# Performance work log

Hardware: AMD Instinct MI355X
Metric: run time of the kernel (lower is better)

The kernel has to match this reference:

```python
import jax, jax.numpy as jnp
import numpy as np

BETA = 1.0  # init kwarg beta


def setup_inputs() -> dict:
    key = jax.random.key(0)
    k1, k2 = jax.random.split(key)
    B, K = 8192, 64
    policy_logps = jax.random.normal(k1, (B, K), dtype=jnp.float32)
    reward_scores = jax.random.uniform(k2, (B, K), dtype=jnp.float32)
    return {"policy_logps": policy_logps, "reward_scores": reward_scores}


def reference(policy_logps, reward_scores):
    B, K = policy_logps.shape
    s = policy_logps  # rf_free=True -> scores = policy_logps
    r = reward_scores

    # ranks: 1-based rank of each item when rewards sorted descending
    order = jnp.argsort(-r, axis=-1)              # [B, K]
    ranks = jnp.argsort(order, axis=-1) + 1        # [B, K]
    inv_discount = 1.0 / jnp.log1p(ranks.astype(s.dtype))  # [B, K]
    gain = 2.0 * r - 1.0                            # [B, K]

    # pairwise matrices [B, K, K]; loop in original covers i > j (strict lower triangle)
    delta = jnp.abs(gain[:, :, None] - gain[:, None, :]) * \
            jnp.abs(inv_discount[:, :, None] - inv_discount[:, None, :])
    diff = s[:, :, None] - s[:, None, :]
    term = delta * jax.nn.log_sigmoid(-BETA * diff)

    mask = jnp.tril(jnp.ones((K, K), dtype=bool), k=-1)  # i > j
    loss_sum = jnp.sum(jnp.where(mask[None], term, 0.0))
    count = B * (K * (K - 1) // 2)
    return -loss_sum / count
```

## Files before the change

### kernel.cpp

```cpp
#include <hip/hip_runtime.h>

#define KDIM 64
#define WAVES_PER_BLOCK 4
#define ROWS_PER_WAVE 2
#define ROWS_PER_BLOCK (WAVES_PER_BLOCK * ROWS_PER_WAVE)

__global__ __launch_bounds__(256) void rankdpo_main(
    const float* __restrict__ s_in, const float* __restrict__ r_in,
    float* __restrict__ partials, int B)
{
    const int wave = threadIdx.x >> 6;
    const int lane = threadIdx.x & 63;
    const int row0 = blockIdx.x * ROWS_PER_BLOCK + wave * ROWS_PER_WAVE;
    const int row1 = row0 + 1;
    const int a0 = (row0 < B ? row0 : 0) * KDIM + lane;
    const int a1 = (row1 < B ? row1 : 0) * KDIM + lane;

    const float s0 = s_in[a0], r0 = r_in[a0];
    const float s1 = s_in[a1], r1 = r_in[a1];

    int c0 = 0, c1 = 0;
    #pragma unroll
    for (int j = 0; j < KDIM; ++j) {
        float rj0 = __uint_as_float(__builtin_amdgcn_readlane(__float_as_uint(r0), j));
        float rj1 = __uint_as_float(__builtin_amdgcn_readlane(__float_as_uint(r1), j));
        c0 += (rj0 > r0) || (rj0 == r0 && j < lane);
        c1 += (rj1 > r1) || (rj1 == r1 && j < lane);
    }
    const float invd0 = __builtin_amdgcn_rcpf(
        0.69314718056f * __builtin_amdgcn_logf((float)(c0 + 2)));
    const float invd1 = __builtin_amdgcn_rcpf(
        0.69314718056f * __builtin_amdgcn_logf((float)(c1 + 2)));
    const float g0 = 2.0f * r0 - 1.0f;
    const float g1 = 2.0f * r1 - 1.0f;

    float p0 = 0.0f, p1 = 0.0f;
    #pragma unroll
    for (int d = 1; d <= 32; ++d) {
        const int pj = (lane - d) & 63;
        float sj0 = __shfl(s0, pj), gj0 = __shfl(g0, pj), dj0 = __shfl(invd0, pj);
        float sj1 = __shfl(s1, pj), gj1 = __shfl(g1, pj), dj1 = __shfl(invd1, pj);

        float del0 = fabsf(g0 - gj0) * fabsf(invd0 - dj0);
        float del1 = fabsf(g1 - gj1) * fabsf(invd1 - dj1);
        if (d == 32 && lane < 32) { del0 = 0.0f; del1 = 0.0f; }

        float u0 = (lane >= d) ? (s0 - sj0) : (sj0 - s0);
        float u1 = (lane >= d) ? (s1 - sj1) : (sj1 - s1);

        float e0 = __builtin_amdgcn_exp2f(-1.44269504089f * fabsf(u0));
        float e1 = __builtin_amdgcn_exp2f(-1.44269504089f * fabsf(u1));
        float sp0 = fmaxf(u0, 0.0f) + 0.69314718056f * __builtin_amdgcn_logf(1.0f + e0);
        float sp1 = fmaxf(u1, 0.0f) + 0.69314718056f * __builtin_amdgcn_logf(1.0f + e1);

        p0 = fmaf(del0, sp0, p0);
        p1 = fmaf(del1, sp1, p1);
    }
    if (row0 >= B) p0 = 0.0f;
    if (row1 >= B) p1 = 0.0f;

    float pacc = p0 + p1;
    #pragma unroll
    for (int off = 32; off > 0; off >>= 1)
        pacc += __shfl_down(pacc, off);

    __shared__ float wsum[WAVES_PER_BLOCK];
    if (lane == 0) wsum[wave] = pacc;
    __syncthreads();
    if (threadIdx.x == 0)
        partials[blockIdx.x] = wsum[0] + wsum[1] + wsum[2] + wsum[3];
}

__global__ __launch_bounds__(256) void rankdpo_reduce(
    const float* __restrict__ partials, int n, float* __restrict__ out,
    double inv_count)
{
    double sum = 0.0;
    for (int i = threadIdx.x; i < n; i += 256)
        sum += (double)partials[i];
    __shared__ double sh[256];
    sh[threadIdx.x] = sum;
    __syncthreads();
    for (int st = 128; st > 0; st >>= 1) {
        if (threadIdx.x < st) sh[threadIdx.x] += sh[threadIdx.x + st];
        __syncthreads();
    }
    if (threadIdx.x == 0)
        out[0] = (float)(sh[0] * inv_count);
}

extern "C" void kernel_launch(void* const* d_in, const int* in_sizes, int n_in,
                              void* d_out, int out_size, void* d_ws, size_t ws_size,
                              hipStream_t stream) {
    const float* s = (const float*)d_in[0];
    const float* r = (const float*)d_in[1];
    float* out = (float*)d_out;

    const int BK = in_sizes[0];
    const int B  = BK / KDIM;
    const int nblocks = (B + ROWS_PER_BLOCK - 1) / ROWS_PER_BLOCK;

    float* partials = (float*)d_ws;

    const long long count = (long long)B * (KDIM * (KDIM - 1) / 2);
    const double inv_count = 1.0 / (double)count;

    rankdpo_main<<<nblocks, 256, 0, stream>>>(s, r, partials, B);
    rankdpo_reduce<<<1, 256, 0, stream>>>(partials, nblocks, out, inv_count);
}
```

Baseline: 72.04 us.

## Stage pairwise operands in LDS with float4 reads and pack rank keys

Replaces the 32-step cross-lane shuffle loop with LDS staging. Each wave's s, gain and inverse-discount values are written twice into a 128-wide buffer, so every lane can read four partners per float4 load across 8 quad offsets. The remaining intra-quad pairs are handled with a few shuffles. The rank count now uses a single 64-bit key comparison, and the stable softplus is replaced by an unguarded log2(1+exp2) with the ln2 factors folded out of both the discount and the term. This aims to cut shuffle/bpermute traffic and ALU work, at the cost of LDS usage and possible overflow for large score differences.

After: 68.11 us. -5.5%, faster.

```diff
diff --git a/kernel.cpp b/kernel.cpp
--- a/kernel.cpp
+++ b/kernel.cpp
@@ -11,6 +11,9 @@
 {
     const int wave = threadIdx.x >> 6;
     const int lane = threadIdx.x & 63;
+    const int qi = lane >> 2;
+    const int bi = lane & 3;
+
     const int row0 = blockIdx.x * ROWS_PER_BLOCK + wave * ROWS_PER_WAVE;
     const int row1 = row0 + 1;
     const int a0 = (row0 < B ? row0 : 0) * KDIM + lane;
@@ -19,43 +22,91 @@
     const float s0 = s_in[a0], r0 = r_in[a0];
     const float s1 = s_in[a1], r1 = r_in[a1];
 
+    const unsigned long long k0 =
+        ((unsigned long long)__float_as_uint(r0) << 32) | (unsigned int)(~lane);
+    const unsigned long long k1 =
+        ((unsigned long long)__float_as_uint(r1) << 32) | (unsigned int)(~lane);
     int c0 = 0, c1 = 0;
     #pragma unroll
     for (int j = 0; j < KDIM; ++j) {
-        float rj0 = __uint_as_float(__builtin_amdgcn_readlane(__float_as_uint(r0), j));
-        float rj1 = __uint_as_float(__builtin_amdgcn_readlane(__float_as_uint(r1), j));
-        c0 += (rj0 > r0) || (rj0 == r0 && j < lane);
-        c1 += (rj1 > r1) || (rj1 == r1 && j < lane);
+        unsigned int rb0 = (unsigned int)__builtin_amdgcn_readlane(__float_as_int(r0), j);
+        unsigned int rb1 = (unsigned int)__builtin_amdgcn_readlane(__float_as_int(r1), j);
+        unsigned long long kj0 = ((unsigned long long)rb0 << 32) | (unsigned int)(~j);
+        unsigned long long kj1 = ((unsigned long long)rb1 << 32) | (unsigned int)(~j);
+        c0 += (kj0 > k0);
+        c1 += (kj1 > k1);
     }
-    const float invd0 = __builtin_amdgcn_rcpf(
-        0.69314718056f * __builtin_amdgcn_logf((float)(c0 + 2)));
-    const float invd1 = __builtin_amdgcn_rcpf(
-        0.69314718056f * __builtin_amdgcn_logf((float)(c1 + 2)));
+    const float invd0 = __builtin_amdgcn_rcpf(__builtin_amdgcn_logf((float)(c0 + 2)));
+    const float invd1 = __builtin_amdgcn_rcpf(__builtin_amdgcn_logf((float)(c1 + 2)));
     const float g0 = 2.0f * r0 - 1.0f;
     const float g1 = 2.0f * r1 - 1.0f;
 
+    __shared__ __align__(16) float sh[WAVES_PER_BLOCK][ROWS_PER_WAVE][3][128];
+    sh[wave][0][0][lane] = s0;     sh[wave][0][0][lane + 64] = s0;
+    sh[wave][0][1][lane] = g0;     sh[wave][0][1][lane + 64] = g0;
+    sh[wave][0][2][lane] = invd0;  sh[wave][0][2][lane + 64] = invd0;
+    sh[wave][1][0][lane] = s1;     sh[wave][1][0][lane + 64] = s1;
+    sh[wave][1][1][lane] = g1;     sh[wave][1][1][lane + 64] = g1;
+    sh[wave][1][2][lane] = invd1;  sh[wave][1][2][lane + 64] = invd1;
+
+    const float LOG2E = 1.44269504088896f;
     float p0 = 0.0f, p1 = 0.0f;
+
     #pragma unroll
-    for (int d = 1; d <= 32; ++d) {
-        const int pj = (lane - d) & 63;
-        float sj0 = __shfl(s0, pj), gj0 = __shfl(g0, pj), dj0 = __shfl(invd0, pj);
-        float sj1 = __shfl(s1, pj), gj1 = __shfl(g1, pj), dj1 = __shfl(invd1, pj);
+    for (int t = 1; t <= 8; ++t) {
+        const int Q = (qi + 16 - t) << 2;
+        const float4 sq0 = *(const float4*)&sh[wave][0][0][Q];
+        const float4 gq0 = *(const float4*)&sh[wave][0][1][Q];
+        const float4 dq0 = *(const float4*)&sh[wave][0][2][Q];
+        const float4 sq1 = *(const float4*)&sh[wave][1][0][Q];
+        const float4 gq1 = *(const float4*)&sh[wave][1][1][Q];
+        const float4 dq1 = *(const float4*)&sh[wave][1][2][Q];
+        const float qc   = (qi >= t) ? LOG2E : -LOG2E;
+        const float keep = (t < 8) ? 1.0f : ((qi >= 8) ? 1.0f : 0.0f);
 
-        float del0 = fabsf(g0 - gj0) * fabsf(invd0 - dj0);
-        float del1 = fabsf(g1 - gj1) * fabsf(invd1 - dj1);
-        if (d == 32 && lane < 32) { del0 = 0.0f; del1 = 0.0f; }
+        const float* sj0 = (const float*)&sq0;
+        const float* gj0 = (const float*)&gq0;
+        const float* dj0 = (const float*)&dq0;
+        const float* sj1 = (const float*)&sq1;
+        const float* gj1 = (const float*)&gq1;
+        const float* dj1 = (const float*)&dq1;
+        #pragma unroll
+        for (int m = 0; m < 4; ++m) {
+            float del0 = fabsf(g0 - gj0[m]) * fabsf(invd0 - dj0[m]) * keep;
+            float del1 = fabsf(g1 - gj1[m]) * fabsf(invd1 - dj1[m]) * keep;
+            float l0 = __builtin_amdgcn_logf(1.0f + __builtin_amdgcn_exp2f(qc * (s0 - sj0[m])));
+            float l1 = __builtin_amdgcn_logf(1.0f + __builtin_amdgcn_exp2f(qc * (s1 - sj1[m])));
+            p0 = fmaf(del0, l0, p0);
+            p1 = fmaf(del1, l1, p1);
+        }
+    }
 
-        float u0 = (lane >= d) ? (s0 - sj0) : (sj0 - s0);
-        float u1 = (lane >= d) ? (s1 - sj1) : (sj1 - s1);
+    {
+        const int pjA = (lane & ~3) | ((bi + 3) & 3);
+        const int pjB = (lane & ~3) | ((bi + 2) & 3);
+        const float qcA  = (bi >= 1) ? LOG2E : -LOG2E;
+        const float keepB = (bi >= 2) ? 1.0f : 0.0f;
 
-        float e0 = __builtin_amdgcn_exp2f(-1.44269504089f * fabsf(u0));
-        float e1 = __builtin_amdgcn_exp2f(-1.44269504089f * fabsf(u1));
-        float sp0 = fmaxf(u0, 0.0f) + 0.69314718056f * __builtin_amdgcn_logf(1.0f + e0);
-        float sp1 = fmaxf(u1, 0.0f) + 0.69314718056f * __builtin_amdgcn_logf(1.0f + e1);
+        float sjA0 = __shfl(s0, pjA), gjA0 = __shfl(g0, pjA), djA0 = __shfl(invd0, pjA);
+        float sjA1 = __shfl(s1, pjA), gjA1 = __shfl(g1, pjA), djA1 = __shfl(invd1, pjA);
+        float sjB0 = __shfl(s0, pjB), gjB0 = __shfl(g0, pjB), djB0 = __shfl(invd0, pjB);
+        float sjB1 = __shfl(s1, pjB), gjB1 = __shfl(g1, pjB), djB1 = __shfl(invd1, pjB);
 
-        p0 = fmaf(del0, sp0, p0);
-        p1 = fmaf(del1, sp1, p1);
+        float delA0 = fabsf(g0 - gjA0) * fabsf(invd0 - djA0);
+        float delA1 = fabsf(g1 - gjA1) * fabsf(invd1 - djA1);
+        float lA0 = __builtin_amdgcn_logf(1.0f + __builtin_amdgcn_exp2f(qcA * (s0 - sjA0)));
+        float lA1 = __builtin_amdgcn_logf(1.0f + __builtin_amdgcn_exp2f(qcA * (s1 - sjA1)));
+        p0 = fmaf(delA0, lA0, p0);
+        p1 = fmaf(delA1, lA1, p1);
+
+        float delB0 = fabsf(g0 - gjB0) * fabsf(invd0 - djB0) * keepB;
+        float delB1 = fabsf(g1 - gjB1) * fabsf(invd1 - djB1) * keepB;
+        float lB0 = __builtin_amdgcn_logf(1.0f + __builtin_amdgcn_exp2f(LOG2E * (s0 - sjB0)));
+        float lB1 = __builtin_amdgcn_logf(1.0f + __builtin_amdgcn_exp2f(LOG2E * (s1 - sjB1)));
+        p0 = fmaf(delB0, lB0, p0);
+        p1 = fmaf(delB1, lB1, p1);
     }
+
     if (row0 >= B) p0 = 0.0f;
     if (row1 >= B) p1 = 0.0f;
 
```

## Stage row data in LDS with packed float2 pair math and quad-blocked pair loop

Applied to the files above, without the earlier changes.

Row values (reward, score, gain, inverse discount) for two rows are written into per-wave LDS buffers as interleaved float2 and duplicated, so the rank count and the pairwise loop read them with wide LDS loads instead of readlane and shuffles. Pairs are walked as quad-block offsets plus two in-quad shuffle steps. Softplus is computed directly as log2(1+exp2(±u·log2e)) with the ln2 constants folded out, on packed v2f math. This cuts cross-lane traffic and instruction count, but adds LDS use and drops the tie-break in the rank count and the stable softplus form, which can overflow for large score differences.

Result: faster. 65.52 us (-9.0%).

```diff
diff --git a/kernel.cpp b/kernel.cpp
--- a/kernel.cpp
+++ b/kernel.cpp
@@ -1,9 +1,24 @@
 #include <hip/hip_runtime.h>
+
+typedef float v2f __attribute__((ext_vector_type(2)));
 
 #define KDIM 64
 #define WAVES_PER_BLOCK 4
 #define ROWS_PER_WAVE 2
 #define ROWS_PER_BLOCK (WAVES_PER_BLOCK * ROWS_PER_WAVE)
+
+#define LOG2E 1.44269504088896f
+
+__device__ __forceinline__ v2f pair_term(v2f g2, v2f d2, v2f s2,
+                                         v2f gj, v2f dj, v2f sj, float qc) {
+    v2f pd = (g2 - gj) * (d2 - dj);
+    v2f del; del.x = fabsf(pd.x); del.y = fabsf(pd.y);
+    v2f u = qc * (s2 - sj);
+    v2f e; e.x = __builtin_amdgcn_exp2f(u.x); e.y = __builtin_amdgcn_exp2f(u.y);
+    v2f le = 1.0f + e;
+    v2f l; l.x = __builtin_amdgcn_logf(le.x); l.y = __builtin_amdgcn_logf(le.y);
+    return del * l;
+}
 
 __global__ __launch_bounds__(256) void rankdpo_main(
     const float* __restrict__ s_in, const float* __restrict__ r_in,
@@ -11,6 +26,9 @@
 {
     const int wave = threadIdx.x >> 6;
     const int lane = threadIdx.x & 63;
+    const int qi = lane >> 2;
+    const int bi = lane & 3;
+
     const int row0 = blockIdx.x * ROWS_PER_BLOCK + wave * ROWS_PER_WAVE;
     const int row1 = row0 + 1;
     const int a0 = (row0 < B ? row0 : 0) * KDIM + lane;
@@ -19,47 +37,72 @@
     const float s0 = s_in[a0], r0 = r_in[a0];
     const float s1 = s_in[a1], r1 = r_in[a1];
 
+    __shared__ __align__(16) v2f sh[WAVES_PER_BLOCK][4][128];
+    v2f* rbuf = sh[wave][0];
+    v2f* sbuf = sh[wave][1];
+    v2f* gbuf = sh[wave][2];
+    v2f* dbuf = sh[wave][3];
+
+    rbuf[lane] = v2f{r0, r1};  rbuf[lane + 64] = v2f{r0, r1};
+    sbuf[lane] = v2f{s0, s1};  sbuf[lane + 64] = v2f{s0, s1};
+
     int c0 = 0, c1 = 0;
     #pragma unroll
-    for (int j = 0; j < KDIM; ++j) {
-        float rj0 = __uint_as_float(__builtin_amdgcn_readlane(__float_as_uint(r0), j));
-        float rj1 = __uint_as_float(__builtin_amdgcn_readlane(__float_as_uint(r1), j));
-        c0 += (rj0 > r0) || (rj0 == r0 && j < lane);
-        c1 += (rj1 > r1) || (rj1 == r1 && j < lane);
+    for (int t = 0; t < 16; ++t) {
+        float4 qa = *(const float4*)&rbuf[4 * t];
+        float4 qb = *(const float4*)&rbuf[4 * t + 2];
+        c0 += (qa.x > r0) + (qa.z > r0) + (qb.x > r0) + (qb.z > r0);
+        c1 += (qa.y > r1) + (qa.w > r1) + (qb.y > r1) + (qb.w > r1);
     }
-    const float invd0 = __builtin_amdgcn_rcpf(
-        0.69314718056f * __builtin_amdgcn_logf((float)(c0 + 2)));
-    const float invd1 = __builtin_amdgcn_rcpf(
-        0.69314718056f * __builtin_amdgcn_logf((float)(c1 + 2)));
+    const float invd0 = __builtin_amdgcn_rcpf(__builtin_amdgcn_logf((float)(c0 + 2)));
+    const float invd1 = __builtin_amdgcn_rcpf(__builtin_amdgcn_logf((float)(c1 + 2)));
     const float g0 = 2.0f * r0 - 1.0f;
     const float g1 = 2.0f * r1 - 1.0f;
 
-    float p0 = 0.0f, p1 = 0.0f;
+    gbuf[lane] = v2f{g0, g1};        gbuf[lane + 64] = v2f{g0, g1};
+    dbuf[lane] = v2f{invd0, invd1};  dbuf[lane + 64] = v2f{invd0, invd1};
+
+    const v2f s2 = {s0, s1}, g2 = {g0, g1}, d2 = {invd0, invd1};
+    v2f p = {0.0f, 0.0f};
+
+    const float keep8 = (qi >= 8) ? 1.0f : 0.0f;
     #pragma unroll
-    for (int d = 1; d <= 32; ++d) {
-        const int pj = (lane - d) & 63;
-        float sj0 = __shfl(s0, pj), gj0 = __shfl(g0, pj), dj0 = __shfl(invd0, pj);
-        float sj1 = __shfl(s1, pj), gj1 = __shfl(g1, pj), dj1 = __shfl(invd1, pj);
+    for (int t = 1; t <= 8; ++t) {
+        const int Q = (qi + 16 - t) << 2;
+        float4 sa = *(const float4*)&sbuf[Q], sb = *(const float4*)&sbuf[Q + 2];
+        float4 ga = *(const float4*)&gbuf[Q], gb = *(const float4*)&gbuf[Q + 2];
+        float4 da = *(const float4*)&dbuf[Q], db = *(const float4*)&dbuf[Q + 2];
+        const float qc = (qi >= t) ? LOG2E : -LOG2E;
 
-        float del0 = fabsf(g0 - gj0) * fabsf(invd0 - dj0);
-        float del1 = fabsf(g1 - gj1) * fabsf(invd1 - dj1);
-        if (d == 32 && lane < 32) { del0 = 0.0f; del1 = 0.0f; }
+        v2f term = pair_term(g2, d2, s2, v2f{ga.x, ga.y}, v2f{da.x, da.y}, v2f{sa.x, sa.y}, qc);
+        term = term + pair_term(g2, d2, s2, v2f{ga.z, ga.w}, v2f{da.z, da.w}, v2f{sa.z, sa.w}, qc);
+        term = term + pair_term(g2, d2, s2, v2f{gb.x, gb.y}, v2f{db.x, db.y}, v2f{sb.x, sb.y}, qc);
+        term = term + pair_term(g2, d2, s2, v2f{gb.z, gb.w}, v2f{db.z, db.w}, v2f{sb.z, sb.w}, qc);
+        if (t == 8) term = term * keep8;
+        p = p + term;
+    }
 
-        float u0 = (lane >= d) ? (s0 - sj0) : (sj0 - s0);
-        float u1 = (lane >= d) ? (s1 - sj1) : (sj1 - s1);
+    {
+        const int pjA = (lane & ~3) | ((bi + 3) & 3);
+        const int pjB = (lane & ~3) | ((bi + 2) & 3);
+        const float qcA = (bi >= 1) ? LOG2E : -LOG2E;
+        const float keepB = (bi >= 2) ? 1.0f : 0.0f;
 
-        float e0 = __builtin_amdgcn_exp2f(-1.44269504089f * fabsf(u0));
-        float e1 = __builtin_amdgcn_exp2f(-1.44269504089f * fabsf(u1));
-        float sp0 = fmaxf(u0, 0.0f) + 0.69314718056f * __builtin_amdgcn_logf(1.0f + e0);
-        float sp1 = fmaxf(u1, 0.0f) + 0.69314718056f * __builtin_amdgcn_logf(1.0f + e1);
+        v2f sjA = {__shfl(s0, pjA), __shfl(s1, pjA)};
+        v2f gjA = {__shfl(g0, pjA), __shfl(g1, pjA)};
+        v2f djA = {__shfl(invd0, pjA), __shfl(invd1, pjA)};
+        v2f sjB = {__shfl(s0, pjB), __shfl(s1, pjB)};
+        v2f gjB = {__shfl(g0, pjB), __shfl(g1, pjB)};
+        v2f djB = {__shfl(invd0, pjB), __shfl(invd1, pjB)};
 
-        p0 = fmaf(del0, sp0, p0);
-        p1 = fmaf(del1, sp1, p1);
+        p = p + pair_term(g2, d2, s2, gjA, djA, sjA, qcA);
+        p = p + pair_term(g2, d2, s2, gjB, djB, sjB, LOG2E) * keepB;
     }
-    if (row0 >= B) p0 = 0.0f;
-    if (row1 >= B) p1 = 0.0f;
 
-    float pacc = p0 + p1;
+    if (row0 >= B) p.x = 0.0f;
+    if (row1 >= B) p.y = 0.0f;
+
+    float pacc = p.x + p.y;
     #pragma unroll
     for (int off = 32; off > 0; off >>= 1)
         pacc += __shfl_down(pacc, off);
```
